# Kernel optimization log

Measured on AMD Instinct MI355X. Metric: run time of the kernel, lower is better.

## Reference

```python
import jax, jax.numpy as jnp
import numpy as np

N = 8192
E = 131072
IN = 512
H = 8
C = 128
HC = H * C
EPS = 1e-5
NEG_SLOPE = 0.2


def _gatv2(x, src, dst, Wl, bl, Wr, br, att, bias):
    """GATv2Conv (PyG semantics, concat=True, self-loops already in src/dst)."""
    n = x.shape[0]
    xl = (x @ Wl + bl).reshape(n, H, C)  # source transform (lin_l)
    xr = (x @ Wr + br).reshape(n, H, C)  # dest transform (lin_r)
    m = xl[src] + xr[dst]                # [E,H,C] per-edge message
    e = jnp.einsum('ehc,hc->eh', jax.nn.leaky_relu(m, NEG_SLOPE), att)  # [E,H]
    # segment softmax over destination nodes
    emax = jax.ops.segment_max(e, dst, num_segments=n)
    w = jnp.exp(e - emax[dst])
    denom = jax.ops.segment_sum(w, dst, num_segments=n)
    alpha = w / denom[dst]               # [E,H]
    out = jax.ops.segment_sum(alpha[:, :, None] * xl[src], dst, num_segments=n)
    return out.reshape(n, HC) + bias


def _bn(x, gamma, beta):
    mu = jnp.mean(x, axis=0)
    var = jnp.mean((x - mu) ** 2, axis=0)
    return (x - mu) * jax.lax.rsqrt(var + EPS) * gamma + beta


def setup_inputs() -> dict:
    key = jax.random.key(0)
    ks = jax.random.split(key, 16)
    s = 0.05
    return {
        'x': jax.random.normal(ks[0], (N, IN), jnp.float32),
        'edge_index': jax.random.randint(ks[1], (2, E), 0, N, jnp.int32),
        'W1l': jax.random.normal(ks[2], (IN, HC), jnp.float32) * s,
        'b1l': jnp.zeros((HC,), jnp.float32),
        'W1r': jax.random.normal(ks[3], (IN, HC), jnp.float32) * s,
        'b1r': jnp.zeros((HC,), jnp.float32),
        'att1': jax.random.normal(ks[4], (H, C), jnp.float32) * s,
        'bias1': jnp.zeros((HC,), jnp.float32),
        'g1': jnp.ones((HC,), jnp.float32),
        'beta1': jnp.zeros((HC,), jnp.float32),
        'W2l': jax.random.normal(ks[5], (HC, HC), jnp.float32) * s,
        'b2l': jnp.zeros((HC,), jnp.float32),
        'W2r': jax.random.normal(ks[6], (HC, HC), jnp.float32) * s,
        'b2r': jnp.zeros((HC,), jnp.float32),
        'att2': jax.random.normal(ks[7], (H, C), jnp.float32) * s,
        'bias2': jnp.zeros((HC,), jnp.float32),
        'g2': jnp.ones((HC,), jnp.float32),
        'beta2': jnp.zeros((HC,), jnp.float32),
    }


def reference(x, edge_index, W1l, b1l, W1r, b1r, att1, bias1, g1, beta1,
              W2l, b2l, W2r, b2r, att2, bias2, g2, beta2):
    n = x.shape[0]
    loops = jnp.arange(n, dtype=edge_index.dtype)
    src = jnp.concatenate([edge_index[0], loops])
    dst = jnp.concatenate([edge_index[1], loops])
    h = _gatv2(x, src, dst, W1l, b1l, W1r, b1r, att1, bias1)
    h = jax.nn.elu(_bn(h, g1, beta1))
    h = _gatv2(h, src, dst, W2l, b2l, W2r, b2r, att2, bias2)
    h = jax.nn.elu(_bn(h, g2, beta2))
    return h
```

## Files before the change

### kernel.cpp

```cpp
#include <hip/hip_runtime.h>
#include <stdint.h>

#define NN     8192
#define NEDGE  131072
#define NETOT  (NEDGE + NN)
#define K_IN   512
#define HC_    1024
#define BNEPS  1e-5f
#define SLOPE  0.2f

typedef __bf16 bf16x8 __attribute__((ext_vector_type(8)));
typedef float  f32x4  __attribute__((ext_vector_type(4)));

__device__ __forceinline__ float bf2f(unsigned short u) {
  union { uint32_t u; float f; } c; c.u = ((uint32_t)u) << 16; return c.f;
}
__device__ __forceinline__ unsigned short f2bf(float f) {
  union { float f; uint32_t u; } c; c.f = f;
  uint32_t r = c.u + 0x7fffu + ((c.u >> 16) & 1u);
  return (unsigned short)(r >> 16);
}
__device__ __forceinline__ void unpack2(uint32_t u, float& lo, float& hi) {
  union { uint32_t u; float f; } a, b;
  a.u = u << 16; b.u = u & 0xffff0000u;
  lo = a.f; hi = b.f;
}

__device__ __forceinline__ void gload16(const void* g, void* l) {
  __builtin_amdgcn_global_load_lds(
      (const __attribute__((address_space(1))) uint32_t*)g,
      (__attribute__((address_space(3))) uint32_t*)l, 16, 0, 0);
}

__global__ __launch_bounds__(256) void k_cvt_bf16(const float* __restrict__ in,
                                                  unsigned short* __restrict__ out, int n4) {
  int i = blockIdx.x * 256 + threadIdx.x;
  if (i >= n4) return;
  float4 v = *(const float4*)&in[(size_t)i * 4];
  ushort4 o;
  o.x = f2bf(v.x); o.y = f2bf(v.y); o.z = f2bf(v.z); o.w = f2bf(v.w);
  *(ushort4*)&out[(size_t)i * 4] = o;
}

__global__ __launch_bounds__(256) void k_transpose_bf16(const float* __restrict__ W,
                                                        unsigned short* __restrict__ Wt,
                                                        int K, int N) {
  __shared__ float tile[32][33];
  int n0 = blockIdx.x * 32, k0 = blockIdx.y * 32;
  int tx = threadIdx.x & 31, ty = threadIdx.x >> 5;
  for (int i = ty; i < 32; i += 8)
    tile[i][tx] = W[(size_t)(k0 + i) * N + n0 + tx];
  __syncthreads();
  for (int i = ty; i < 32; i += 8)
    Wt[(size_t)(n0 + i) * K + k0 + tx] = f2bf(tile[tx][i]);
}

__global__ __launch_bounds__(256) void k_hist(const int* __restrict__ ei, int* __restrict__ cnt) {
  int i = blockIdx.x * 256 + threadIdx.x;
  if (i >= NETOT) return;
  int d = (i < NEDGE) ? ei[NEDGE + i] : (i - NEDGE);
  atomicAdd(&cnt[d], 1);
}

__global__ __launch_bounds__(256) void k_scan(const int* __restrict__ cnt,
                                              int* __restrict__ rowptr,
                                              int* __restrict__ cursor) {
  __shared__ int part[256];
  int t = threadIdx.x;
  int base = t * 32;
  int s = 0;
  for (int i = 0; i < 32; ++i) s += cnt[base + i];
  part[t] = s;
  __syncthreads();
  for (int off = 1; off < 256; off <<= 1) {
    int u = (t >= off) ? part[t - off] : 0;
    __syncthreads();
    part[t] += u;
    __syncthreads();
  }
  int run = part[t] - s;
  for (int i = 0; i < 32; ++i) {
    rowptr[base + i] = run;
    cursor[base + i] = run;
    run += cnt[base + i];
  }
  if (t == 255) rowptr[NN] = run;
}

__global__ __launch_bounds__(256) void k_scatter(const int* __restrict__ ei,
                                                 int* __restrict__ cursor,
                                                 int* __restrict__ srcs) {
  int i = blockIdx.x * 256 + threadIdx.x;
  if (i >= NETOT) return;
  int s, d;
  if (i < NEDGE) { s = ei[i]; d = ei[NEDGE + i]; }
  else           { s = d = i - NEDGE; }
  int pos = atomicAdd(&cursor[d], 1);
  srcs[pos] = s;
}

__global__ __launch_bounds__(256) void k_gemm2_bt(const unsigned short* __restrict__ A,
                                                  const unsigned short* __restrict__ BtL,
                                                  const unsigned short* __restrict__ BtR,
                                                  const float* __restrict__ biasL,
                                                  const float* __restrict__ biasR,
                                                  unsigned short* __restrict__ CL,
                                                  unsigned short* __restrict__ CR,
                                                  int M, int K) {
  __shared__ unsigned short lA[128 * 64];
  __shared__ unsigned short lB[128 * 64];
  const int bx = blockIdx.x;
  const unsigned short* Bt = (bx < 8) ? BtL : BtR;
  const float* bias        = (bx < 8) ? biasL : biasR;
  unsigned short* C        = (bx < 8) ? CL : CR;
  const int n0 = (bx & 7) * 128;

  const int tid = threadIdx.x;
  const int l   = tid & 63;
  const int w   = tid >> 6;
  const int wm  = w >> 1, wn = w & 1;
  const int m0  = blockIdx.y * 128;
  const int l15 = l & 15, l4 = l >> 4;

  const f32x4 vzero = {0.f, 0.f, 0.f, 0.f};
  f32x4 acc[4][4];
#pragma unroll
  for (int i = 0; i < 4; ++i)
#pragma unroll
    for (int j = 0; j < 4; ++j) acc[i][j] = vzero;

  for (int k0 = 0; k0 < K; k0 += 64) {
#pragma unroll
    for (int i = 0; i < 4; ++i) {
      int ch = i * 256 + tid;
      int row = ch >> 3, gk = ch & 7;
      int sgk = gk ^ (row & 7);
      gload16(&A[(size_t)(m0 + row) * K + k0 + sgk * 8], &lA[ch * 8]);
    }
#pragma unroll
    for (int i = 0; i < 4; ++i) {
      int ch = i * 256 + tid;
      int row = ch >> 3, gk = ch & 7;
      int sgk = gk ^ (row & 7);
      gload16(&Bt[(size_t)(n0 + row) * K + k0 + sgk * 8], &lB[ch * 8]);
    }
    __syncthreads();
#pragma unroll
    for (int kk = 0; kk < 2; ++kk) {
      bf16x8 af[4], bfr[4];
#pragma unroll
      for (int f = 0; f < 4; ++f) {
        int ar = wm * 64 + f * 16 + l15;
        int ag = (kk * 4 + l4) ^ (ar & 7);
        af[f] = *(const bf16x8*)&lA[ar * 64 + ag * 8];
        int br = wn * 64 + f * 16 + l15;
        int bg = (kk * 4 + l4) ^ (br & 7);
        bfr[f] = *(const bf16x8*)&lB[br * 64 + bg * 8];
      }
#pragma unroll
      for (int fm = 0; fm < 4; ++fm)
#pragma unroll
        for (int fn = 0; fn < 4; ++fn)
          acc[fm][fn] = __builtin_amdgcn_mfma_f32_16x16x32_bf16(af[fm], bfr[fn], acc[fm][fn], 0, 0, 0);
    }
    __syncthreads();
  }

#pragma unroll
  for (int fm = 0; fm < 4; ++fm) {
#pragma unroll
    for (int fn = 0; fn < 4; ++fn) {
      int col = n0 + wn * 64 + fn * 16 + l15;
      float bv = bias[col];
#pragma unroll
      for (int j = 0; j < 4; ++j) {
        int row = m0 + wm * 64 + fm * 16 + l4 * 4 + j;
        C[(size_t)row * HC_ + col] = f2bf(acc[fm][fn][j] + bv);
      }
    }
  }
}

__global__ __launch_bounds__(256) void k_edge_agg(const unsigned short* __restrict__ XL,
                                                  const unsigned short* __restrict__ XR,
                                                  const float* __restrict__ att,
                                                  const float* __restrict__ bias,
                                                  const int* __restrict__ rowptr,
                                                  const int* __restrict__ srcs,
                                                  float* __restrict__ out) {
  const int d   = blockIdx.x;
  const int tid = threadIdx.x;
  const int g   = tid >> 6;
  const int l   = tid & 63;
  const int c0  = l * 16;

  float attv[16], xrv[16];
  {
    const float4* ap = (const float4*)&att[c0];
#pragma unroll
    for (int q = 0; q < 4; ++q) {
      float4 v = ap[q];
      attv[q * 4 + 0] = v.x; attv[q * 4 + 1] = v.y;
      attv[q * 4 + 2] = v.z; attv[q * 4 + 3] = v.w;
    }
    const uint4* rp = (const uint4*)&XR[(size_t)d * HC_ + c0];
    uint4 u0 = rp[0], u1 = rp[1];
    unpack2(u0.x, xrv[0], xrv[1]);  unpack2(u0.y, xrv[2], xrv[3]);
    unpack2(u0.z, xrv[4], xrv[5]);  unpack2(u0.w, xrv[6], xrv[7]);
    unpack2(u1.x, xrv[8], xrv[9]);  unpack2(u1.y, xrv[10], xrv[11]);
    unpack2(u1.z, xrv[12], xrv[13]); unpack2(u1.w, xrv[14], xrv[15]);
  }

  float acc[16];
#pragma unroll
  for (int j = 0; j < 16; ++j) acc[j] = 0.f;
  float den = 0.f;

  const int beg = rowptr[d], end = rowptr[d + 1];
  for (int i = beg + g; i < end; i += 4) {
    const int s = srcs[i];
    const uint4* rp = (const uint4*)&XL[(size_t)s * HC_ + c0];
    uint4 u0 = rp[0], u1 = rp[1];
    float x[16];
    unpack2(u0.x, x[0], x[1]);   unpack2(u0.y, x[2], x[3]);
    unpack2(u0.z, x[4], x[5]);   unpack2(u0.w, x[6], x[7]);
    unpack2(u1.x, x[8], x[9]);   unpack2(u1.y, x[10], x[11]);
    unpack2(u1.z, x[12], x[13]); unpack2(u1.w, x[14], x[15]);
    float p = 0.f;
#pragma unroll
    for (int j = 0; j < 16; ++j) {
      float m  = x[j] + xrv[j];
      float lr = fmaxf(m, SLOPE * m);
      p = fmaf(lr, attv[j], p);
    }
    p += __shfl_xor(p, 1);
    p += __shfl_xor(p, 2);
    p += __shfl_xor(p, 4);
    float wgt = __expf(p);
    den += wgt;
#pragma unroll
    for (int j = 0; j < 16; ++j) acc[j] = fmaf(wgt, x[j], acc[j]);
  }

  __shared__ float sacc[4][64][17];
  __shared__ float sden[4][64];
#pragma unroll
  for (int j = 0; j < 16; ++j) sacc[g][l][j] = acc[j];
  sden[g][l] = den;
  __syncthreads();

  const int c  = tid * 4;
  const int hl = (c >> 7) * 8;
  float dtot = sden[0][hl] + sden[1][hl] + sden[2][hl] + sden[3][hl];
  float inv  = 1.0f / dtot;
  float4 bv  = *(const float4*)&bias[c];
  float o[4];
#pragma unroll
  for (int j = 0; j < 4; ++j) {
    int cc = c + j, ll = cc >> 4, jj = cc & 15;
    float s = sacc[0][ll][jj] + sacc[1][ll][jj] + sacc[2][ll][jj] + sacc[3][ll][jj];
    o[j] = s * inv;
  }
  float4 ov = {o[0] + bv.x, o[1] + bv.y, o[2] + bv.z, o[3] + bv.w};
  *(float4*)&out[(size_t)d * HC_ + c] = ov;
}

__global__ __launch_bounds__(256) void k_colstats(const float* __restrict__ X,
                                                  float* __restrict__ stats) {
  int col = blockIdx.x * 256 + threadIdx.x;
  int r0 = blockIdx.y * 128;
  float s = 0.f, q = 0.f;
  for (int r = r0; r < r0 + 128; ++r) {
    float v = X[(size_t)r * HC_ + col];
    s += v;
    q += v * v;
  }
  atomicAdd(&stats[col], s);
  atomicAdd(&stats[HC_ + col], q);
}

template <bool OUT_BF16>
__global__ __launch_bounds__(256) void k_bn_elu(const float* __restrict__ X,
                                                const float* __restrict__ stats,
                                                const float* __restrict__ gamma,
                                                const float* __restrict__ beta,
                                                void* __restrict__ outp) {
  size_t idx = (size_t)blockIdx.x * 256 + threadIdx.x;
  size_t e0 = idx * 4;
  int col = (int)(e0 & (HC_ - 1));
  float4 xv = *(const float4*)&X[e0];
  float xs[4] = {xv.x, xv.y, xv.z, xv.w};
  float os[4];
  const float rn = 1.0f / (float)NN;
#pragma unroll
  for (int j = 0; j < 4; ++j) {
    int c = col + j;
    float mu = stats[c] * rn;
    float var = stats[HC_ + c] * rn - mu * mu;
    float v = (xs[j] - mu) * rsqrtf(var + BNEPS) * gamma[c] + beta[c];
    os[j] = v > 0.f ? v : (__expf(v) - 1.f);
  }
  if (OUT_BF16) {
    ushort4 o;
    o.x = f2bf(os[0]); o.y = f2bf(os[1]); o.z = f2bf(os[2]); o.w = f2bf(os[3]);
    *(ushort4*)&((unsigned short*)outp)[e0] = o;
  } else {
    float4 o = {os[0], os[1], os[2], os[3]};
    *(float4*)&((float*)outp)[e0] = o;
  }
}

extern "C" void kernel_launch(void* const* d_in, const int* in_sizes, int n_in,
                              void* d_out, int out_size, void* d_ws, size_t ws_size,
                              hipStream_t stream) {
  const float* x     = (const float*)d_in[0];
  const int*   ei    = (const int*)d_in[1];
  const float* W1l   = (const float*)d_in[2];
  const float* b1l   = (const float*)d_in[3];
  const float* W1r   = (const float*)d_in[4];
  const float* b1r   = (const float*)d_in[5];
  const float* att1  = (const float*)d_in[6];
  const float* bias1 = (const float*)d_in[7];
  const float* g1    = (const float*)d_in[8];
  const float* be1   = (const float*)d_in[9];
  const float* W2l   = (const float*)d_in[10];
  const float* b2l   = (const float*)d_in[11];
  const float* W2r   = (const float*)d_in[12];
  const float* b2r   = (const float*)d_in[13];
  const float* att2  = (const float*)d_in[14];
  const float* bias2 = (const float*)d_in[15];
  const float* g2    = (const float*)d_in[16];
  const float* be2   = (const float*)d_in[17];
  float* out = (float*)d_out;

  char* wsb = (char*)d_ws;
  size_t o = 0;
  auto alloc = [&](size_t b) {
    void* p = wsb + o;
    o = (o + b + 255) & ~(size_t)255;
    return p;
  };
  unsigned short* xbf   = (unsigned short*)alloc((size_t)NN * K_IN * 2);
  unsigned short* w1lT  = (unsigned short*)alloc((size_t)K_IN * HC_ * 2);
  unsigned short* w1rT  = (unsigned short*)alloc((size_t)K_IN * HC_ * 2);
  unsigned short* w2lT  = (unsigned short*)alloc((size_t)HC_ * HC_ * 2);
  unsigned short* w2rT  = (unsigned short*)alloc((size_t)HC_ * HC_ * 2);
  unsigned short* XL    = (unsigned short*)alloc((size_t)NN * HC_ * 2);
  unsigned short* XR    = (unsigned short*)alloc((size_t)NN * HC_ * 2);
  unsigned short* h1bf  = (unsigned short*)alloc((size_t)NN * HC_ * 2);
  int* cnt     = (int*)alloc((size_t)NN * 4);
  int* rowptr  = (int*)alloc((size_t)(NN + 1) * 4);
  int* cursor  = (int*)alloc((size_t)NN * 4);
  int* srcs    = (int*)alloc((size_t)NETOT * 4);
  float* stats = (float*)alloc((size_t)2 * HC_ * 4);

  hipMemsetAsync(cnt, 0, (size_t)NN * 4, stream);
  hipMemsetAsync(stats, 0, (size_t)2 * HC_ * 4, stream);

  k_cvt_bf16<<<(NN * K_IN / 4 + 255) / 256, 256, 0, stream>>>(x, xbf, NN * K_IN / 4);
  k_transpose_bf16<<<dim3(HC_ / 32, K_IN / 32), 256, 0, stream>>>(W1l, w1lT, K_IN, HC_);
  k_transpose_bf16<<<dim3(HC_ / 32, K_IN / 32), 256, 0, stream>>>(W1r, w1rT, K_IN, HC_);
  k_transpose_bf16<<<dim3(HC_ / 32, HC_ / 32), 256, 0, stream>>>(W2l, w2lT, HC_, HC_);
  k_transpose_bf16<<<dim3(HC_ / 32, HC_ / 32), 256, 0, stream>>>(W2r, w2rT, HC_, HC_);

  k_hist<<<(NETOT + 255) / 256, 256, 0, stream>>>(ei, cnt);
  k_scan<<<1, 256, 0, stream>>>(cnt, rowptr, cursor);
  k_scatter<<<(NETOT + 255) / 256, 256, 0, stream>>>(ei, cursor, srcs);

  const dim3 ggrid2(16, NN / 128);

  k_gemm2_bt<<<ggrid2, 256, 0, stream>>>(xbf, w1lT, w1rT, b1l, b1r, XL, XR, NN, K_IN);
  k_edge_agg<<<NN, 256, 0, stream>>>(XL, XR, att1, bias1, rowptr, srcs, out);
  k_colstats<<<dim3(HC_ / 256, NN / 128), 256, 0, stream>>>(out, stats);
  k_bn_elu<true><<<NN * HC_ / 4 / 256, 256, 0, stream>>>(out, stats, g1, be1, h1bf);

  k_gemm2_bt<<<ggrid2, 256, 0, stream>>>(h1bf, w2lT, w2rT, b2l, b2r, XL, XR, NN, HC_);
  k_edge_agg<<<NN, 256, 0, stream>>>(XL, XR, att2, bias2, rowptr, srcs, out);
  hipMemsetAsync(stats, 0, (size_t)2 * HC_ * 4, stream);
  k_colstats<<<dim3(HC_ / 256, NN / 128), 256, 0, stream>>>(out, stats);
  k_bn_elu<false><<<NN * HC_ / 4 / 256, 256, 0, stream>>>(out, stats, g2, be2, out);
}
```

Baseline: 263.2 us.

## Use 256x256 double-buffered GEMM tiles with interleaved XL/XR output layout

Replaces the 128x128 single-buffered GEMM with a 256x256 tile, 512-thread kernel that double-buffers LDS loads with explicit waitcnt/barrier pipelining and XCD-aware block mapping. The two weight matrices are concatenated into one transposed buffer so a single GEMM writes an interleaved [N, 2048] XL|XR output, which the edge aggregation kernel now reads with stride 2048. The aim is more operand reuse per tile and overlapping global loads with MFMA work. In exchange it uses 128KB of LDS per block and many more registers, which limits occupancy, and the interleaved layout gives gathered rows a larger stride.

```diff
diff --git a/kernel.cpp b/kernel.cpp
--- a/kernel.cpp
+++ b/kernel.cpp
@@ -6,6 +6,7 @@
 #define NETOT  (NEDGE + NN)
 #define K_IN   512
 #define HC_    1024
+#define NOUT   2048
 #define BNEPS  1e-5f
 #define SLOPE  0.2f
 
@@ -99,90 +100,112 @@
   srcs[pos] = s;
 }
 
-__global__ __launch_bounds__(256) void k_gemm2_bt(const unsigned short* __restrict__ A,
-                                                  const unsigned short* __restrict__ BtL,
-                                                  const unsigned short* __restrict__ BtR,
-                                                  const float* __restrict__ biasL,
-                                                  const float* __restrict__ biasR,
-                                                  unsigned short* __restrict__ CL,
-                                                  unsigned short* __restrict__ CR,
-                                                  int M, int K) {
-  __shared__ unsigned short lA[128 * 64];
-  __shared__ unsigned short lB[128 * 64];
-  const int bx = blockIdx.x;
-  const unsigned short* Bt = (bx < 8) ? BtL : BtR;
-  const float* bias        = (bx < 8) ? biasL : biasR;
-  unsigned short* C        = (bx < 8) ? CL : CR;
-  const int n0 = (bx & 7) * 128;
+__global__ __launch_bounds__(512, 2) void k_gemm256(const unsigned short* __restrict__ A,
+                                                    const unsigned short* __restrict__ Bt,
+                                                    const float* __restrict__ biasL,
+                                                    const float* __restrict__ biasR,
+                                                    unsigned short* __restrict__ C,
+                                                    int K) {
+  __shared__ unsigned short lA[2][256 * 64];
+  __shared__ unsigned short lB[2][256 * 64];
+
+  const int bid = blockIdx.x;
+  const int xcd = bid & 7, idx = bid >> 3;
+  const int m0 = (xcd * 4 + (idx & 3)) * 256;
+  const int n0 = (idx >> 2) * 256;
 
   const int tid = threadIdx.x;
   const int l   = tid & 63;
-  const int w   = tid >> 6;
-  const int wm  = w >> 1, wn = w & 1;
-  const int m0  = blockIdx.y * 128;
+  const int wv  = tid >> 6;
+  const int wm  = wv >> 2, wn = wv & 3;
   const int l15 = l & 15, l4 = l >> 4;
 
+  const int row0 = tid >> 3;
+  const int sgk  = (tid & 7) ^ (row0 & 7);
+  const size_t aoff0 = (size_t)(m0 + row0) * K + sgk * 8;
+  const size_t boff0 = (size_t)(n0 + row0) * K + sgk * 8;
+  const int ldsch = tid * 8;
+
   const f32x4 vzero = {0.f, 0.f, 0.f, 0.f};
-  f32x4 acc[4][4];
-#pragma unroll
-  for (int i = 0; i < 4; ++i)
+  f32x4 acc[8][4];
+#pragma unroll
+  for (int i = 0; i < 8; ++i)
 #pragma unroll
     for (int j = 0; j < 4; ++j) acc[i][j] = vzero;
 
-  for (int k0 = 0; k0 < K; k0 += 64) {
-#pragma unroll
-    for (int i = 0; i < 4; ++i) {
-      int ch = i * 256 + tid;
-      int row = ch >> 3, gk = ch & 7;
-      int sgk = gk ^ (row & 7);
-      gload16(&A[(size_t)(m0 + row) * K + k0 + sgk * 8], &lA[ch * 8]);
-    }
-#pragma unroll
-    for (int i = 0; i < 4; ++i) {
-      int ch = i * 256 + tid;
-      int row = ch >> 3, gk = ch & 7;
-      int sgk = gk ^ (row & 7);
-      gload16(&Bt[(size_t)(n0 + row) * K + k0 + sgk * 8], &lB[ch * 8]);
-    }
-    __syncthreads();
+  auto stage = [&](int kt, int buf) {
+    const int k0 = kt * 64;
+#pragma unroll
+    for (int i = 0; i < 4; ++i)
+      gload16(&A[aoff0 + (size_t)i * 64 * K + k0], &lA[buf][ldsch + i * 4096]);
+#pragma unroll
+    for (int i = 0; i < 4; ++i)
+      gload16(&Bt[boff0 + (size_t)i * 64 * K + k0], &lB[buf][ldsch + i * 4096]);
+  };
+
+  auto compute = [&](int buf) {
+    __builtin_amdgcn_s_setprio(1);
 #pragma unroll
     for (int kk = 0; kk < 2; ++kk) {
-      bf16x8 af[4], bfr[4];
+      bf16x8 af[8], bfr[4];
+#pragma unroll
+      for (int f = 0; f < 8; ++f) {
+        int r = wm * 128 + f * 16 + l15;
+        int g = (kk * 4 + l4) ^ (r & 7);
+        af[f] = *(const bf16x8*)&lA[buf][r * 64 + g * 8];
+      }
 #pragma unroll
       for (int f = 0; f < 4; ++f) {
-        int ar = wm * 64 + f * 16 + l15;
-        int ag = (kk * 4 + l4) ^ (ar & 7);
-        af[f] = *(const bf16x8*)&lA[ar * 64 + ag * 8];
-        int br = wn * 64 + f * 16 + l15;
-        int bg = (kk * 4 + l4) ^ (br & 7);
-        bfr[f] = *(const bf16x8*)&lB[br * 64 + bg * 8];
+        int r = wn * 64 + f * 16 + l15;
+        int g = (kk * 4 + l4) ^ (r & 7);
+        bfr[f] = *(const bf16x8*)&lB[buf][r * 64 + g * 8];
       }
 #pragma unroll
-      for (int fm = 0; fm < 4; ++fm)
+      for (int fm = 0; fm < 8; ++fm)
 #pragma unroll
         for (int fn = 0; fn < 4; ++fn)
           acc[fm][fn] = __builtin_amdgcn_mfma_f32_16x16x32_bf16(af[fm], bfr[fn], acc[fm][fn], 0, 0, 0);
     }
-    __syncthreads();
-  }
-
-#pragma unroll
-  for (int fm = 0; fm < 4; ++fm) {
+    __builtin_amdgcn_s_setprio(0);
+  };
+
+  const int NT = K >> 6;
+  stage(0, 0);
+  stage(1, 1);
+  int cur = 0;
+  for (int kt = 0; kt < NT - 1; ++kt) {
+    asm volatile("s_waitcnt vmcnt(8)" ::: "memory");
+    __builtin_amdgcn_s_barrier();
+    asm volatile("" ::: "memory");
+    compute(cur);
+    asm volatile("" ::: "memory");
+    __builtin_amdgcn_s_barrier();
+    asm volatile("" ::: "memory");
+    if (kt < NT - 2) stage(kt + 2, cur);
+    cur ^= 1;
+  }
+  asm volatile("s_waitcnt vmcnt(0)" ::: "memory");
+  __builtin_amdgcn_s_barrier();
+  asm volatile("" ::: "memory");
+  compute(cur);
+
+  const float* bias = (n0 < HC_) ? biasL : (biasR - HC_);
+#pragma unroll
+  for (int fm = 0; fm < 8; ++fm) {
 #pragma unroll
     for (int fn = 0; fn < 4; ++fn) {
       int col = n0 + wn * 64 + fn * 16 + l15;
       float bv = bias[col];
 #pragma unroll
       for (int j = 0; j < 4; ++j) {
-        int row = m0 + wm * 64 + fm * 16 + l4 * 4 + j;
-        C[(size_t)row * HC_ + col] = f2bf(acc[fm][fn][j] + bv);
+        int row = m0 + wm * 128 + fm * 16 + l4 * 4 + j;
+        C[(size_t)row * NOUT + col] = f2bf(acc[fm][fn][j] + bv);
       }
     }
   }
 }
 
-__global__ __launch_bounds__(256) void k_edge_agg(const unsigned short* __restrict__ XL,
-                                                  const unsigned short* __restrict__ XR,
+__global__ __launch_bounds__(256) void k_edge_agg(const unsigned short* __restrict__ XLR,
                                                   const float* __restrict__ att,
                                                   const float* __restrict__ bias,
                                                   const int* __restrict__ rowptr,
@@ -203,7 +226,7 @@
       attv[q * 4 + 0] = v.x; attv[q * 4 + 1] = v.y;
       attv[q * 4 + 2] = v.z; attv[q * 4 + 3] = v.w;
     }
-    const uint4* rp = (const uint4*)&XR[(size_t)d * HC_ + c0];
+    const uint4* rp = (const uint4*)&XLR[(size_t)d * NOUT + HC_ + c0];
     uint4 u0 = rp[0], u1 = rp[1];
     unpack2(u0.x, xrv[0], xrv[1]);  unpack2(u0.y, xrv[2], xrv[3]);
     unpack2(u0.z, xrv[4], xrv[5]);  unpack2(u0.w, xrv[6], xrv[7]);
@@ -219,7 +242,7 @@
   const int beg = rowptr[d], end = rowptr[d + 1];
   for (int i = beg + g; i < end; i += 4) {
     const int s = srcs[i];
-    const uint4* rp = (const uint4*)&XL[(size_t)s * HC_ + c0];
+    const uint4* rp = (const uint4*)&XLR[(size_t)s * NOUT + c0];
     uint4 u0 = rp[0], u1 = rp[1];
     float x[16];
     unpack2(u0.x, x[0], x[1]);   unpack2(u0.y, x[2], x[3]);
@@ -340,14 +363,11 @@
     o = (o + b + 255) & ~(size_t)255;
     return p;
   };
-  unsigned short* xbf   = (unsigned short*)alloc((size_t)NN * K_IN * 2);
-  unsigned short* w1lT  = (unsigned short*)alloc((size_t)K_IN * HC_ * 2);
-  unsigned short* w1rT  = (unsigned short*)alloc((size_t)K_IN * HC_ * 2);
-  unsigned short* w2lT  = (unsigned short*)alloc((size_t)HC_ * HC_ * 2);
-  unsigned short* w2rT  = (unsigned short*)alloc((size_t)HC_ * HC_ * 2);
-  unsigned short* XL    = (unsigned short*)alloc((size_t)NN * HC_ * 2);
-  unsigned short* XR    = (unsigned short*)alloc((size_t)NN * HC_ * 2);
-  unsigned short* h1bf  = (unsigned short*)alloc((size_t)NN * HC_ * 2);
+  unsigned short* xbf  = (unsigned short*)alloc((size_t)NN * K_IN * 2);
+  unsigned short* wT1  = (unsigned short*)alloc((size_t)NOUT * K_IN * 2);
+  unsigned short* wT2  = (unsigned short*)alloc((size_t)NOUT * HC_ * 2);
+  unsigned short* XLR  = (unsigned short*)alloc((size_t)NN * NOUT * 2);
+  unsigned short* h1bf = (unsigned short*)alloc((size_t)NN * HC_ * 2);
   int* cnt     = (int*)alloc((size_t)NN * 4);
   int* rowptr  = (int*)alloc((size_t)(NN + 1) * 4);
   int* cursor  = (int*)alloc((size_t)NN * 4);
@@ -358,24 +378,22 @@
   hipMemsetAsync(stats, 0, (size_t)2 * HC_ * 4, stream);
 
   k_cvt_bf16<<<(NN * K_IN / 4 + 255) / 256, 256, 0, stream>>>(x, xbf, NN * K_IN / 4);
-  k_transpose_bf16<<<dim3(HC_ / 32, K_IN / 32), 256, 0, stream>>>(W1l, w1lT, K_IN, HC_);
-  k_transpose_bf16<<<dim3(HC_ / 32, K_IN / 32), 256, 0, stream>>>(W1r, w1rT, K_IN, HC_);
-  k_transpose_bf16<<<dim3(HC_ / 32, HC_ / 32), 256, 0, stream>>>(W2l, w2lT, HC_, HC_);
-  k_transpose_bf16<<<dim3(HC_ / 32, HC_ / 32), 256, 0, stream>>>(W2r, w2rT, HC_, HC_);
+  k_transpose_bf16<<<dim3(HC_ / 32, K_IN / 32), 256, 0, stream>>>(W1l, wT1, K_IN, HC_);
+  k_transpose_bf16<<<dim3(HC_ / 32, K_IN / 32), 256, 0, stream>>>(W1r, wT1 + (size_t)HC_ * K_IN, K_IN, HC_);
+  k_transpose_bf16<<<dim3(HC_ / 32, HC_ / 32), 256, 0, stream>>>(W2l, wT2, HC_, HC_);
+  k_transpose_bf16<<<dim3(HC_ / 32, HC_ / 32), 256, 0, stream>>>(W2r, wT2 + (size_t)HC_ * HC_, HC_, HC_);
 
   k_hist<<<(NETOT + 255) / 256, 256, 0, stream>>>(ei, cnt);
   k_scan<<<1, 256, 0, stream>>>(cnt, rowptr, cursor);
   k_scatter<<<(NETOT + 255) / 256, 256, 0, stream>>>(ei, cursor, srcs);
 
-  const dim3 ggrid2(16, NN / 128);
-
-  k_gemm2_bt<<<ggrid2, 256, 0, stream>>>(xbf, w1lT, w1rT, b1l, b1r, XL, XR, NN, K_IN);
-  k_edge_agg<<<NN, 256, 0, stream>>>(XL, XR, att1, bias1, rowptr, srcs, out);
+  k_gemm256<<<256, 512, 0, stream>>>(xbf, wT1, b1l, b1r, XLR, K_IN);
+  k_edge_agg<<<NN, 256, 0, stream>>>(XLR, att1, bias1, rowptr, srcs, out);
   k_colstats<<<dim3(HC_ / 256, NN / 128), 256, 0, stream>>>(out, stats);
   k_bn_elu<true><<<NN * HC_ / 4 / 256, 256, 0, stream>>>(out, stats, g1, be1, h1bf);
 
-  k_gemm2_bt<<<ggrid2, 256, 0, stream>>>(h1bf, w2lT, w2rT, b2l, b2r, XL, XR, NN, HC_);
-  k_edge_agg<<<NN, 256, 0, stream>>>(XL, XR, att2, bias2, rowptr, srcs, out);
+  k_gemm256<<<256, 512, 0, stream>>>(h1bf, wT2, b2l, b2r, XLR, HC_);
+  k_edge_agg<<<NN, 256, 0, stream>>>(XLR, att2, bias2, rowptr, srcs, out);
   hipMemsetAsync(stats, 0, (size_t)2 * HC_ * 4, stream);
   k_colstats<<<dim3(HC_ / 256, NN / 128), 256, 0, stream>>>(out, stats);
   k_bn_elu<false><<<NN * HC_ / 4 / 256, 256, 0, stream>>>(out, stats, g2, be2, out);
```

New measurement: 253.3 us. 3.7% less time.
